# Performance work log

Hardware: AMD Instinct MI355X
Metric: run time of the kernel (lower is better)

## Reference

```python
import jax, jax.numpy as jnp
import numpy as np

B, C, V, K, COUT = 4, 64, 40962, 9, 64  # graph_level 6 -> 10*4^6+2 = 40962 vertices


def setup_inputs() -> dict:
    key = jax.random.key(0)
    k1, k2, k3, k4, k5 = jax.random.split(key, 5)
    return {
        "x": jax.random.normal(k1, (B, C, V), dtype=jnp.float32),
        "index": jax.random.randint(k2, (V, K), 0, V),  # per-vertex neighbor ids
        "itp_mat": jax.random.normal(k3, (V, K, K), dtype=jnp.float32) * 0.2,
        "conv_w": jax.random.normal(k4, (COUT, C, 1, K), dtype=jnp.float32) * 0.05,
        "conv_b": jax.random.normal(k5, (COUT,), dtype=jnp.float32) * 0.05,
    }


def reference(x, index, itp_mat, conv_w, conv_b):
    # x: [B, C, V]. Original: permute(2,0,1) -> [V,B,C]; gather neighbors -> [V,K,B,C];
    # select_index = arange(V) (stride=1, select_index=None), so selection is identity.
    g = jnp.transpose(x, (2, 0, 1))[index]          # [V, K, B, C] neighbor gather
    g = jnp.transpose(g, (2, 3, 0, 1))              # [B, C, V, K]
    # Interploate: batched per-vertex matmul [B,C,V,1,K] @ [V,K,K] -> [B,C,V,1,K]
    itp = jnp.einsum('bcvk,vkj->bcvj', g, itp_mat)  # [B, C, V, K]
    # Conv2d with kernel (1, K): contracts C and K per vertex -> [B, COUT, V]
    out = jnp.einsum('bcvj,ocj->bov', itp, conv_w[:, :, 0, :]) + conv_b[None, :, None]
    # sparse_reset: scatter into zeros at select_index = arange(V) -> identity
    return out
```

## Files before the change

kernel.cpp:

```cpp
#include <hip/hip_runtime.h>
#include <hip/hip_bf16.h>

#define VN 40962
#define NG 10241
#define LDA_B 1168
#define OFF_C 18688
#define LDS_TOT 23040
#define XT_BYTES (VN * 512)

typedef float f32x4 __attribute__((ext_vector_type(4)));
typedef float f32x2 __attribute__((ext_vector_type(2)));
typedef __bf16 bf16x8 __attribute__((ext_vector_type(8)));

__global__ __launch_bounds__(256) void k_transpose(const float* __restrict__ x,
                                                   __bf16* __restrict__ xt) {
    __shared__ __bf16 tile[64][65];
    const int v0 = blockIdx.x * 64;
    const int t0 = blockIdx.y * 64;
    const int lane = threadIdx.x & 63;
    const int sub = threadIdx.x >> 6;

#pragma unroll
    for (int r = 0; r < 16; ++r) {
        const int t = t0 + r * 4 + sub;
        const int v = v0 + lane;
        float val = (v < VN) ? x[(size_t)t * VN + v] : 0.f;
        tile[r * 4 + sub][lane] = (__bf16)val;
    }
    __syncthreads();
#pragma unroll
    for (int r = 0; r < 16; ++r) {
        const int vv = r * 4 + sub;
        const int v = v0 + vv;
        if (v < VN) xt[(size_t)v * 256 + t0 + lane] = tile[lane][vv];
    }
}

__global__ __launch_bounds__(64) void k_wprep(const float* __restrict__ conv_w,
                                              __bf16* __restrict__ wf) {
    const int id = blockIdx.x;
    const int ks = id % 18;
    const int w  = id / 18;
    const int lane = threadIdx.x;
    const int o  = w * 16 + (lane & 15);
    const int kb = (lane >> 4) * 8;
    const float* wrow = conv_w + (size_t)o * 576 + ks * 32 + kb;
    bf16x8 f;
#pragma unroll
    for (int e = 0; e < 8; ++e) f[e] = (__bf16)wrow[e];
    *(bf16x8*)(wf + ((size_t)id * 64 + lane) * 8) = f;
}

__global__ __launch_bounds__(256) void k_fused(const __bf16* __restrict__ xt,
                                               const int* __restrict__ index,
                                               const float* __restrict__ itp_mat,
                                               const __bf16* __restrict__ wf,
                                               const float* __restrict__ conv_b,
                                               float* __restrict__ out) {
    __shared__ char smem[LDS_TOT];

    const int tid  = threadIdx.x;
    const int lane = tid & 63;
    const int w    = tid >> 6;
    const int l16  = lane & 15;
    const int g4   = lane >> 4;
    const int v0   = blockIdx.x * 4;

#pragma unroll 2
    for (int vv = 0; vv < 4; ++vv) {
        const int v  = v0 + vv;
        const int vm = (v < VN) ? v : VN - 1;
        const int* idxv = index + (size_t)vm * 9;
        const float* am = itp_mat + (size_t)vm * 81;
        float gv[9];
#pragma unroll
        for (int k = 0; k < 9; ++k)
            gv[k] = (float)xt[(size_t)idxv[k] * 256 + tid];
        float s[9];
#pragma unroll
        for (int j = 0; j < 9; ++j) s[j] = 0.f;
#pragma unroll
        for (int k = 0; k < 9; ++k) {
            const float gk = gv[k];
#pragma unroll
            for (int j = 0; j < 9; ++j) s[j] += gk * am[k * 9 + j];
        }
        __bf16* rowp = (__bf16*)(smem + (vv * 4 + w) * LDA_B) + lane * 9;
#pragma unroll
        for (int j = 0; j < 9; ++j) rowp[j] = (__bf16)s[j];
    }
    __syncthreads();

    f32x4 acc = {0.f, 0.f, 0.f, 0.f};
    {
        const char* ar = smem + l16 * LDA_B + g4 * 16;
        const __bf16* wfp = wf + ((size_t)(w * 18) * 64 + lane) * 8;
#pragma unroll
        for (int ks = 0; ks < 18; ++ks) {
            bf16x8 a  = *(const bf16x8*)(ar + ks * 64);
            bf16x8 wb = *(const bf16x8*)(wfp + (size_t)ks * 512);
            acc = __builtin_amdgcn_mfma_f32_16x16x32_bf16(a, wb, acc, 0, 0, 0);
        }
    }
    {
        float* c_lds = (float*)(smem + OFF_C);
#pragma unroll
        for (int r = 0; r < 4; ++r)
            c_lds[(g4 * 4 + r) * 68 + w * 16 + l16] = acc[r];
    }
    __syncthreads();

    {
        const float* c_lds = (const float*)(smem + OFF_C);
        const float bias_v = conv_b[lane];
        float vals[4];
#pragma unroll
        for (int vv = 0; vv < 4; ++vv)
            vals[vv] = c_lds[(vv * 4 + w) * 68 + lane] + bias_v;
        float* op = out + (size_t)tid * VN + v0;
        const int vleft = VN - v0;
        if (vleft >= 4) {
            *(f32x2*)op       = f32x2{vals[0], vals[1]};
            *(f32x2*)(op + 2) = f32x2{vals[2], vals[3]};
        } else {
#pragma unroll
            for (int vv = 0; vv < 4; ++vv) if (vv < vleft) op[vv] = vals[vv];
        }
    }
}

extern "C" void kernel_launch(void* const* d_in, const int* in_sizes, int n_in,
                              void* d_out, int out_size, void* d_ws, size_t ws_size,
                              hipStream_t stream) {
    const float* x       = (const float*)d_in[0];
    const int*   index   = (const int*)d_in[1];
    const float* itp_mat = (const float*)d_in[2];
    const float* conv_w  = (const float*)d_in[3];
    const float* conv_b  = (const float*)d_in[4];
    float* out = (float*)d_out;

    __bf16* xt = (__bf16*)d_ws;
    __bf16* wfrag = (__bf16*)((char*)d_ws + XT_BYTES);

    dim3 tgrid((VN + 63) / 64, 4, 1);
    k_transpose<<<tgrid, 256, 0, stream>>>(x, xt);
    k_wprep<<<72, 64, 0, stream>>>(conv_w, wfrag);
    k_fused<<<NG, 256, 0, stream>>>(xt, index, itp_mat, wfrag, conv_b, out);
}
```

Baseline: 97.35 us.

## Gather bf16 pairs per thread, pack LDS writes, and alias C tile to cut LDS

Each thread now handles two adjacent channels of one batch for two vertices. It loads neighbor pairs as 32-bit words, unpacks the bf16 values with bit operations, and writes packed 32-bit words into the A tile. The C staging buffer now reuses the A tile region after an extra barrier, which shrinks LDS, and the launch bounds request 8 blocks per CU. The aim is fewer and wider gather loads and LDS stores plus higher occupancy, at the cost of one more sync and more live accumulator registers per thread.

```diff
diff --git a/kernel.cpp b/kernel.cpp
--- a/kernel.cpp
+++ b/kernel.cpp
@@ -4,13 +4,23 @@
 #define VN 40962
 #define NG 10241
 #define LDA_B 1168
-#define OFF_C 18688
-#define LDS_TOT 23040
+#define LDS_TOT 18688
 #define XT_BYTES (VN * 512)
 
 typedef float f32x4 __attribute__((ext_vector_type(4)));
 typedef float f32x2 __attribute__((ext_vector_type(2)));
 typedef __bf16 bf16x8 __attribute__((ext_vector_type(8)));
+
+__device__ __forceinline__ float bf16lo(unsigned u) {
+    return __builtin_bit_cast(float, u << 16);
+}
+__device__ __forceinline__ float bf16hi(unsigned u) {
+    return __builtin_bit_cast(float, u & 0xffff0000u);
+}
+__device__ __forceinline__ unsigned bf16b(float x) {
+    __bf16 h = (__bf16)x;
+    return (unsigned)__builtin_bit_cast(unsigned short, h);
+}
 
 __global__ __launch_bounds__(256) void k_transpose(const float* __restrict__ x,
                                                    __bf16* __restrict__ xt) {
@@ -51,12 +61,12 @@
     *(bf16x8*)(wf + ((size_t)id * 64 + lane) * 8) = f;
 }
 
-__global__ __launch_bounds__(256) void k_fused(const __bf16* __restrict__ xt,
-                                               const int* __restrict__ index,
-                                               const float* __restrict__ itp_mat,
-                                               const __bf16* __restrict__ wf,
-                                               const float* __restrict__ conv_b,
-                                               float* __restrict__ out) {
+__global__ __launch_bounds__(256, 8) void k_fused(const __bf16* __restrict__ xt,
+                                                  const int* __restrict__ index,
+                                                  const float* __restrict__ itp_mat,
+                                                  const __bf16* __restrict__ wf,
+                                                  const float* __restrict__ conv_b,
+                                                  float* __restrict__ out) {
     __shared__ char smem[LDS_TOT];
 
     const int tid  = threadIdx.x;
@@ -66,28 +76,46 @@
     const int g4   = lane >> 4;
     const int v0   = blockIdx.x * 4;
 
-#pragma unroll 2
-    for (int vv = 0; vv < 4; ++vv) {
+    const int p  = tid & 31;
+    const int bb = (tid >> 5) & 3;
+    const int vh = tid >> 7;
+
+#pragma unroll
+    for (int vs = 0; vs < 2; ++vs) {
+        const int vv = vh + 2 * vs;
         const int v  = v0 + vv;
         const int vm = (v < VN) ? v : VN - 1;
         const int* idxv = index + (size_t)vm * 9;
         const float* am = itp_mat + (size_t)vm * 81;
-        float gv[9];
+
+        unsigned gd[9];
 #pragma unroll
         for (int k = 0; k < 9; ++k)
-            gv[k] = (float)xt[(size_t)idxv[k] * 256 + tid];
-        float s[9];
+            gd[k] = *(const unsigned*)(xt + (size_t)idxv[k] * 256 + bb * 64 + 2 * p);
+
+        float s0[9], s1[9];
 #pragma unroll
-        for (int j = 0; j < 9; ++j) s[j] = 0.f;
+        for (int j = 0; j < 9; ++j) { s0[j] = 0.f; s1[j] = 0.f; }
 #pragma unroll
         for (int k = 0; k < 9; ++k) {
-            const float gk = gv[k];
+            const float glo = bf16lo(gd[k]);
+            const float ghi = bf16hi(gd[k]);
 #pragma unroll
-            for (int j = 0; j < 9; ++j) s[j] += gk * am[k * 9 + j];
+            for (int j = 0; j < 9; ++j) {
+                const float a = am[k * 9 + j];
+                s0[j] += glo * a;
+                s1[j] += ghi * a;
+            }
         }
-        __bf16* rowp = (__bf16*)(smem + (vv * 4 + w) * LDA_B) + lane * 9;
+
+        unsigned* wp = (unsigned*)(smem + (size_t)(vv * 4 + bb) * LDA_B + 36 * p);
 #pragma unroll
-        for (int j = 0; j < 9; ++j) rowp[j] = (__bf16)s[j];
+        for (int q = 0; q < 9; ++q) {
+            const int t0i = 2 * q, t1i = 2 * q + 1;
+            const float e0 = (t0i < 9) ? s0[t0i] : s1[t0i - 9];
+            const float e1 = (t1i < 9) ? s0[t1i] : s1[t1i - 9];
+            wp[q] = bf16b(e0) | (bf16b(e1) << 16);
+        }
     }
     __syncthreads();
 
@@ -102,8 +130,10 @@
             acc = __builtin_amdgcn_mfma_f32_16x16x32_bf16(a, wb, acc, 0, 0, 0);
         }
     }
+    __syncthreads();
+
     {
-        float* c_lds = (float*)(smem + OFF_C);
+        float* c_lds = (float*)smem;
 #pragma unroll
         for (int r = 0; r < 4; ++r)
             c_lds[(g4 * 4 + r) * 68 + w * 16 + l16] = acc[r];
@@ -111,7 +141,7 @@
     __syncthreads();
 
     {
-        const float* c_lds = (const float*)(smem + OFF_C);
+        const float* c_lds = (const float*)smem;
         const float bias_v = conv_b[lane];
         float vals[4];
 #pragma unroll
```

New measurement: 231.2 us. +137.5%, slower.
